# Kernel optimization log

Measured on AMD Instinct MI355X. Metric: run time of the kernel, lower is better.

The kernel has to match this reference:

```python
import jax, jax.numpy as jnp
import numpy as np

B, N, C = 8, 4096, 512
NH, R = 8, 4
EPS = 1e-5

def setup_inputs() -> dict:
    key = jax.random.key(0)
    ks = jax.random.split(key, 6)
    s = lambda k, shape: jax.random.normal(k, shape, jnp.float32) * 0.02
    return {
        'x': jax.random.normal(ks[0], (B, N, C), jnp.float32),
        'Wq': s(ks[1], (C, C)), 'bq': jnp.zeros((C,), jnp.float32),
        'Wkv': s(ks[2], (C, 2 * C)), 'bkv': jnp.zeros((2 * C,), jnp.float32),
        'Wp': s(ks[3], (C, C)), 'bp': jnp.zeros((C,), jnp.float32),
        'Wsr': s(ks[4], (C, C, R, R)), 'bsr': jnp.zeros((C,), jnp.float32),
        'gamma': jnp.ones((C,), jnp.float32), 'beta': jnp.zeros((C,), jnp.float32),
        'H': 64, 'W': 64,
    }

def reference(x, Wq, bq, Wkv, bkv, Wp, bp, Wsr, bsr, gamma, beta, H, W):
    b, n, c = x.shape
    nh = NH
    hd = c // nh
    scale = hd ** -0.5
    # Q projection -> [B, nh, N, hd]
    q = (x @ Wq + bq).reshape(b, n, nh, hd).transpose(0, 2, 1, 3)
    # spatial reduction of KV input: Conv2d(k=stride=R), NCHW
    x_sp = x.transpose(0, 2, 1).reshape(b, c, H, W)
    xr = jax.lax.conv_general_dilated(
        x_sp, Wsr, window_strides=(R, R), padding='VALID',
        dimension_numbers=('NCHW', 'OIHW', 'NCHW')) + bsr[None, :, None, None]
    nr = (H // R) * (W // R)
    xr = xr.reshape(b, c, nr).transpose(0, 2, 1)  # [B, Nr, C]
    # LayerNorm over channels
    mu = xr.mean(-1, keepdims=True)
    var = xr.var(-1, keepdims=True)
    xr = (xr - mu) / jnp.sqrt(var + EPS) * gamma + beta
    # KV projection -> k, v: [B, nh, Nr, hd]
    kv = (xr @ Wkv + bkv).reshape(b, nr, 2, nh, hd)
    k = kv[:, :, 0].transpose(0, 2, 1, 3)
    v = kv[:, :, 1].transpose(0, 2, 1, 3)
    # attention
    attn = jax.nn.softmax(jnp.einsum('bhnd,bhmd->bhnm', q, k) * scale, axis=-1)
    out = jnp.einsum('bhnm,bhmd->bhnd', attn, v).transpose(0, 2, 1, 3).reshape(b, n, c)
    return out @ Wp + bp
```

## Files before the change

kernel.cpp:

```cpp
#include <hip/hip_runtime.h>
#include <stdint.h>

typedef __attribute__((ext_vector_type(8))) short bf16x8;
typedef __attribute__((ext_vector_type(4))) float f32x4;
typedef __attribute__((ext_vector_type(2))) unsigned u32x2;

#define MFMA16(a,b,c) __builtin_amdgcn_mfma_f32_16x16x32_bf16(a,b,c,0,0,0)

typedef const __attribute__((address_space(1))) void GV;
typedef __attribute__((address_space(3))) void LV;

static __device__ __forceinline__ void gload16(const void* g, void* l) {
  __builtin_amdgcn_global_load_lds((GV*)g, (LV*)l, 16, 0, 0);
}

static __device__ __forceinline__ unsigned short f2bf(float f) {
  union { float f; unsigned u; } x; x.f = f;
  unsigned r = x.u + 0x7FFFu + ((x.u >> 16) & 1u);
  return (unsigned short)(r >> 16);
}

static __device__ __forceinline__ float fast_exp2(float x) {
#if __has_builtin(__builtin_amdgcn_exp2f)
  return __builtin_amdgcn_exp2f(x);
#else
  return __expf(x * 0.6931471805599453f);
#endif
}

__global__ __launch_bounds__(256) void pack_x_kernel(
    const float* __restrict__ x, unsigned short* __restrict__ xb) {
  int i = blockIdx.x * 256 + threadIdx.x;
  float4 v = ((const float4*)x)[i];
  unsigned a0 = f2bf(v.x), a1 = f2bf(v.y), a2 = f2bf(v.z), a3 = f2bf(v.w);
  uint2 pk; pk.x = a0 | (a1 << 16); pk.y = a2 | (a3 << 16);
  ((uint2*)xb)[i] = pk;
}

__global__ __launch_bounds__(256) void pack_w_kernel(
    const float* __restrict__ Wq, const float* __restrict__ Wkv,
    const float* __restrict__ Wp, const float* __restrict__ Wsr,
    unsigned short* __restrict__ wqt, unsigned short* __restrict__ wkvt,
    unsigned short* __restrict__ wpt, unsigned short* __restrict__ wsrt) {
  int idx = blockIdx.x * 256 + threadIdx.x;
  if (idx < 262144) {
    int n = idx >> 9, k = idx & 511;
    wqt[idx] = f2bf(Wq[k * 512 + n]);
  } else if (idx < 786432) {
    int j = idx - 262144; int n = j >> 9, k = j & 511;
    wkvt[j] = f2bf(Wkv[k * 1024 + n]);
  } else if (idx < 1048576) {
    int j = idx - 786432; int n = j >> 9, k = j & 511;
    wpt[j] = f2bf(Wp[k * 512 + n]);
  } else {
    int j = idx - 1048576;
    int oc = j >> 13, rem = j & 8191;
    int r12 = rem >> 9, ic = rem & 511;
    wsrt[j] = f2bf(Wsr[oc * 8192 + ic * 16 + r12]);
  }
}

template<int WM, int WN, int MREP, int NREP, int MODE, bool CONV, bool SWZ>
__global__ __launch_bounds__(256) void gemm_bf16(
    const unsigned short* __restrict__ A, const unsigned short* __restrict__ Bt,
    const float* __restrict__ bias, void* __restrict__ outp,
    unsigned short* __restrict__ out_k, unsigned short* __restrict__ out_v,
    int M, int N, int K, int lda, int Ksub) {
  constexpr int BM = WM * MREP * 16;
  constexpr int BN = WN * NREP * 16;
  constexpr int BK = 64;
  constexpr int ABYTES = BM * BK * 2;
  constexpr int BBYTES = BN * BK * 2;
  __shared__ unsigned short lds_a[2 * BM * BK];
  __shared__ unsigned short lds_b[2 * BN * BK];
  const int tid = threadIdx.x;
  const int lane = tid & 63, w = tid >> 6;
  const int wr = w / WN, wc = w % WN;
  const int l15 = lane & 15, lhi = lane >> 4;
  const int xmask = (l15 & 7) << 4;
  const int smask = ((tid >> 3) & 7) << 3;
  int mt, nt_;
  if constexpr (SWZ) {
    int lin = blockIdx.x + blockIdx.y * gridDim.x;
    int nwg = gridDim.x * gridDim.y;
    int cpx = nwg >> 3;
    int s = (lin & 7) * cpx + (lin >> 3);
    int gdy = gridDim.y;
    mt = s / gdy; nt_ = s - mt * gdy;
  } else { mt = blockIdx.x; nt_ = blockIdx.y; }
  const int m0 = mt * BM;
  const int n0 = nt_ * BN;
  const int kbeg = blockIdx.z * Ksub;

  f32x4 acc[MREP][NREP] = {};
  constexpr int AR = ABYTES / 4096;
  constexpr int BR = BBYTES / 4096;
  constexpr int NL = AR + BR;

  auto stage = [&](int buf, int k0) {
    #pragma unroll
    for (int r = 0; r < AR; ++r) {
      int o = r * 4096 + tid * 16;
      int row = o >> 7;
      int kc = (((o & 127) >> 1)) ^ smask;
      const unsigned short* src;
      if constexpr (CONV) {
        int m = m0 + row;
        int bb = m >> 8, pix = m & 255;
        int oh = pix >> 4, ow = pix & 15;
        int r12 = k0 >> 9;
        int icc = (k0 & 511) + kc;
        int r1 = r12 >> 2, r2 = r12 & 3;
        int nn = (oh * 4 + r1) * 64 + ow * 4 + r2;
        src = A + ((size_t)(bb * 4096 + nn)) * 512 + icc;
      } else {
        src = A + (size_t)(m0 + row) * lda + k0 + kc;
      }
      gload16(src, (char*)lds_a + buf * ABYTES + r * 4096 + w * 1024);
    }
    #pragma unroll
    for (int r = 0; r < BR; ++r) {
      int o = r * 4096 + tid * 16;
      int row = o >> 7;
      int kc = (((o & 127) >> 1)) ^ smask;
      const unsigned short* src = Bt + (size_t)(n0 + row) * K + k0 + kc;
      gload16(src, (char*)lds_b + buf * BBYTES + r * 4096 + w * 1024);
    }
  };

  auto waitn = [&]() {
    if constexpr (NL == 4)      asm volatile("s_waitcnt vmcnt(4)" ::: "memory");
    else if constexpr (NL == 6) asm volatile("s_waitcnt vmcnt(6)" ::: "memory");
    else                        asm volatile("s_waitcnt vmcnt(8)" ::: "memory");
  };

  auto compute = [&](int buf) {
    const char* pa = (const char*)lds_a + buf * ABYTES;
    const char* pb = (const char*)lds_b + buf * BBYTES;
    #pragma unroll
    for (int kk = 0; kk < BK; kk += 32) {
      bf16x8 af[MREP], bfr[NREP];
      #pragma unroll
      for (int m = 0; m < MREP; ++m)
        af[m] = *(const bf16x8*)(pa + (wr * MREP * 16 + m * 16 + l15) * (BK * 2)
                                 + (((kk << 1) + (lhi << 4)) ^ xmask));
      #pragma unroll
      for (int n = 0; n < NREP; ++n)
        bfr[n] = *(const bf16x8*)(pb + (wc * NREP * 16 + n * 16 + l15) * (BK * 2)
                                  + (((kk << 1) + (lhi << 4)) ^ xmask));
      __builtin_amdgcn_s_setprio(1);
      #pragma unroll
      for (int m = 0; m < MREP; ++m)
        #pragma unroll
        for (int n = 0; n < NREP; ++n)
          acc[m][n] = MFMA16(af[m], bfr[n], acc[m][n]);
      __builtin_amdgcn_s_setprio(0);
    }
  };

  const int nsteps = Ksub / BK;
  stage(0, kbeg);
  int buf = 0;
  for (int t = 0; t < nsteps; ++t) {
    if (t + 1 < nsteps) {
      stage(buf ^ 1, kbeg + (t + 1) * BK);
      waitn();
    } else {
      asm volatile("s_waitcnt vmcnt(0)" ::: "memory");
    }
    __builtin_amdgcn_s_barrier();
    compute(buf);
    __builtin_amdgcn_s_barrier();
    buf ^= 1;
  }

  #pragma unroll
  for (int m = 0; m < MREP; ++m) {
    #pragma unroll
    for (int n = 0; n < NREP; ++n) {
      #pragma unroll
      for (int r = 0; r < 4; ++r) {
        int gm = m0 + wr * MREP * 16 + m * 16 + lhi * 4 + r;
        int gn = n0 + wc * NREP * 16 + n * 16 + l15;
        if constexpr (MODE == 0) {
          float v = acc[m][n][r] + bias[gn];
          ((float*)outp)[(size_t)gm * N + gn] = v;
        } else if constexpr (MODE == 3) {
          ((float*)outp)[((size_t)blockIdx.z * M + gm) * N + gn] = acc[m][n][r];
        } else if constexpr (MODE == 4) {
          float v = (acc[m][n][r] + bias[gn]) * 0.18033688011112042f;
          int b_ = gm >> 12, n_ = gm & 4095;
          int hh = gn >> 6, d = gn & 63;
          int qt = n_ >> 4, half = d >> 5, dd = d & 31;
          int ln = (n_ & 15) | ((dd >> 3) << 4);
          ((unsigned short*)outp)[(size_t)(b_ * 8 + hh) * 262144 +
              (qt * 2 + half) * 512 + ln * 8 + (d & 7)] = f2bf(v);
        } else {
          float v = acc[m][n][r] + bias[gn];
          unsigned short bv = f2bf(v);
          int bb = gm >> 8, nr = gm & 255;
          if (gn < 512) {
            int hh = gn >> 6, d = gn & 63;
            int t_ = nr >> 4, half = d >> 5, dd = d & 31;
            int ln = (nr & 15) | ((dd >> 3) << 4);
            out_k[(size_t)(bb * 8 + hh) * 16384 +
                  (t_ * 2 + half) * 512 + ln * 8 + (d & 7)] = bv;
          } else {
            int c = gn - 512;
            int hh = c >> 6, d = c & 63;
            int nn = d >> 4, cl = d & 15;
            int ks = nr >> 5, lh = (nr >> 3) & 3;
            out_v[(size_t)(bb * 8 + hh) * 16384 +
                  (nn * 8 + ks) * 512 + (cl | (lh << 4)) * 8 + (nr & 7)] = bv;
          }
        }
      }
    }
  }
}

__global__ __launch_bounds__(64) void ln_kernel(
    const float* __restrict__ part, const float* __restrict__ bsr,
    const float* __restrict__ gamma, const float* __restrict__ beta,
    unsigned short* __restrict__ xln) {
  const int row = blockIdx.x, lane = threadIdx.x;
  float vv[8];
  #pragma unroll
  for (int j = 0; j < 8; ++j) vv[j] = bsr[lane * 8 + j];
  #pragma unroll
  for (int p = 0; p < 4; ++p) {
    const float* pp = part + ((size_t)p * 2048 + row) * 512 + lane * 8;
    float4 a0 = *(const float4*)pp;
    float4 a1 = *(const float4*)(pp + 4);
    vv[0] += a0.x; vv[1] += a0.y; vv[2] += a0.z; vv[3] += a0.w;
    vv[4] += a1.x; vv[5] += a1.y; vv[6] += a1.z; vv[7] += a1.w;
  }
  float s = 0.f, s2 = 0.f;
  #pragma unroll
  for (int j = 0; j < 8; ++j) { s += vv[j]; s2 += vv[j] * vv[j]; }
  #pragma unroll
  for (int m_ = 1; m_ < 64; m_ <<= 1) { s += __shfl_xor(s, m_); s2 += __shfl_xor(s2, m_); }
  float mean = s * (1.f / 512.f);
  float var = s2 * (1.f / 512.f) - mean * mean;
  float inv = rsqrtf(var + 1e-5f);
  #pragma unroll
  for (int j = 0; j < 8; ++j) {
    int c = lane * 8 + j;
    xln[(size_t)row * 512 + c] = f2bf((vv[j] - mean) * inv * gamma[c] + beta[c]);
  }
}

__global__ __launch_bounds__(512, 4) void attn_kernel(
    const unsigned short* __restrict__ qfrag, const unsigned short* __restrict__ kfrag,
    const unsigned short* __restrict__ vfrag, unsigned short* __restrict__ aout) {
  __shared__ unsigned short k_lds[16384];
  __shared__ unsigned short v_lds[16384];
  const int tid = threadIdx.x, lane = tid & 63, w = tid >> 6;
  const int l15 = lane & 15;
  const int b = blockIdx.z, h = blockIdx.y;
  const int bh = b * 8 + h;
  const char* kb_ = (const char*)(kfrag + (size_t)bh * 16384);
  const char* vb_ = (const char*)(vfrag + (size_t)bh * 16384);
  #pragma unroll
  for (int r = 0; r < 4; ++r) {
    gload16(kb_ + r * 8192 + tid * 16, (char*)k_lds + r * 8192 + w * 1024);
    gload16(vb_ + r * 8192 + tid * 16, (char*)v_lds + r * 8192 + w * 1024);
  }
  const int qt = blockIdx.x * 8 + w;
  const unsigned short* qbase = qfrag + (size_t)bh * 262144 + (size_t)qt * 1024;
  bf16x8 qf0 = *(const bf16x8*)(qbase + lane * 8);
  bf16x8 qf1 = *(const bf16x8*)(qbase + 512 + lane * 8);
  __syncthreads();

  f32x4 st[16];
  #pragma unroll
  for (int t = 0; t < 16; ++t) {
    bf16x8 kf0 = *(const bf16x8*)&k_lds[t * 1024 + lane * 8];
    bf16x8 kf1 = *(const bf16x8*)&k_lds[t * 1024 + 512 + lane * 8];
    f32x4 a = {0.f, 0.f, 0.f, 0.f};
    a = MFMA16(kf0, qf0, a);
    a = MFMA16(kf1, qf1, a);
    st[t] = a;
  }

  float sum = 0.f;
  unsigned pk2[16][2];
  #pragma unroll
  for (int t = 0; t < 16; ++t) {
    float p0 = fast_exp2(st[t][0]), p1 = fast_exp2(st[t][1]);
    float p2 = fast_exp2(st[t][2]), p3 = fast_exp2(st[t][3]);
    sum += (p0 + p1) + (p2 + p3);
    unsigned r0, r1;
    asm("v_cvt_pk_bf16_f32 %0, %1, %2" : "=v"(r0) : "v"(p0), "v"(p1));
    asm("v_cvt_pk_bf16_f32 %0, %1, %2" : "=v"(r1) : "v"(p2), "v"(p3));
    pk2[t][0] = r0; pk2[t][1] = r1;
  }
  sum += __shfl_xor(sum, 16);
  sum += __shfl_xor(sum, 32);
  float invs = 1.f / sum;

  const int lhi_ = lane >> 4;
  const int srcA = l15 + (((2 * lhi_) & 3) << 4);
  const int srcB = l15 + (((2 * lhi_ + 1) & 3) << 4);
  const bool hi2 = lhi_ >= 2;
  f32x4 o[4] = {};
  #pragma unroll
  for (int ks = 0; ks < 8; ++ks) {
    union { unsigned u[4]; bf16x8 v; } pu;
    unsigned A0 = __shfl(pk2[2 * ks][0], srcA),     A0b = __shfl(pk2[2 * ks][1], srcA);
    unsigned A1 = __shfl(pk2[2 * ks + 1][0], srcA), A1b = __shfl(pk2[2 * ks + 1][1], srcA);
    unsigned B0 = __shfl(pk2[2 * ks][0], srcB),     B0b = __shfl(pk2[2 * ks][1], srcB);
    unsigned B1 = __shfl(pk2[2 * ks + 1][0], srcB), B1b = __shfl(pk2[2 * ks + 1][1], srcB);
    pu.u[0] = hi2 ? A1 : A0;  pu.u[1] = hi2 ? A1b : A0b;
    pu.u[2] = hi2 ? B1 : B0;  pu.u[3] = hi2 ? B1b : B0b;
    #pragma unroll
    for (int n = 0; n < 4; ++n) {
      bf16x8 vf = *(const bf16x8*)&v_lds[(n * 8 + ks) * 512 + lane * 8];
      o[n] = MFMA16(vf, pu.v, o[n]);
    }
  }

  const int q0 = blockIdx.x * 128;
  const int lhi = lane >> 4;
  #pragma unroll
  for (int n = 0; n < 4; ++n) {
    float a0 = o[n][0] * invs, a1 = o[n][1] * invs;
    float a2 = o[n][2] * invs, a3 = o[n][3] * invs;
    unsigned w0, w1;
    asm("v_cvt_pk_bf16_f32 %0, %1, %2" : "=v"(w0) : "v"(a0), "v"(a1));
    asm("v_cvt_pk_bf16_f32 %0, %1, %2" : "=v"(w1) : "v"(a2), "v"(a3));
    u32x2 pr; pr[0] = w0; pr[1] = w1;
    size_t base = (size_t)(b * 4096 + q0 + w * 16 + l15) * 512 + h * 64 + n * 16 + lhi * 4;
    *(u32x2*)(aout + base) = pr;
  }
}

extern "C" void kernel_launch(void* const* d_in, const int* in_sizes, int n_in,
                              void* d_out, int out_size, void* d_ws, size_t ws_size,
                              hipStream_t stream) {
  const float* x     = (const float*)d_in[0];
  const float* Wq    = (const float*)d_in[1];
  const float* bq    = (const float*)d_in[2];
  const float* Wkv   = (const float*)d_in[3];
  const float* bkv   = (const float*)d_in[4];
  const float* Wp    = (const float*)d_in[5];
  const float* bp    = (const float*)d_in[6];
  const float* Wsr   = (const float*)d_in[7];
  const float* bsr   = (const float*)d_in[8];
  const float* gamma = (const float*)d_in[9];
  const float* beta  = (const float*)d_in[10];

  char* ws = (char*)d_ws;
  unsigned short* xb    = (unsigned short*)(ws + 0);
  float*          part  = (float*)(ws + 33554432);
  unsigned short* qfrag = (unsigned short*)(ws + 33554432);
  unsigned short* wqt   = (unsigned short*)(ws + 67108864);
  unsigned short* wkvt  = (unsigned short*)(ws + 67633152);
  unsigned short* wpt   = (unsigned short*)(ws + 68681728);
  unsigned short* wsrt  = (unsigned short*)(ws + 69206016);
  unsigned short* xln   = (unsigned short*)(ws + 77594624);
  unsigned short* kfrag = (unsigned short*)(ws + 79691776);
  unsigned short* vfrag = (unsigned short*)(ws + 81788928);
  unsigned short* aout  = xb;

  pack_x_kernel<<<16384, 256, 0, stream>>>(x, xb);
  pack_w_kernel<<<20480, 256, 0, stream>>>(Wq, Wkv, Wp, Wsr, wqt, wkvt, wpt, wsrt);
  gemm_bf16<2, 2, 2, 2, 3, true, false><<<dim3(32, 8, 4), 256, 0, stream>>>(
      xb, wsrt, nullptr, part, nullptr, nullptr, 2048, 512, 8192, 512, 2048);
  ln_kernel<<<2048, 64, 0, stream>>>(part, bsr, gamma, beta, xln);
  gemm_bf16<2, 2, 2, 4, 2, false, false><<<dim3(32, 8, 1), 256, 0, stream>>>(
      xln, wkvt, bkv, nullptr, kfrag, vfrag, 2048, 1024, 512, 512, 512);
  gemm_bf16<2, 2, 4, 4, 4, false, true><<<dim3(256, 4, 1), 256, 0, stream>>>(
      xb, wqt, bq, qfrag, nullptr, nullptr, 32768, 512, 512, 512, 512);
  attn_kernel<<<dim3(32, 8, 8), 512, 0, stream>>>(qfrag, kfrag, vfrag, aout);
  gemm_bf16<2, 2, 4, 4, 0, false, true><<<dim3(256, 4, 1), 256, 0, stream>>>(
      aout, wpt, bp, (float*)d_out, nullptr, nullptr, 32768, 512, 512, 512, 512);
}
```

Before: 168.7 us.

## Merge pack kernels, fuse Q and KV projections, retile conv split-K

Combines the x and weight packing into one launch and transposes the weights through LDS tiles so both reads and writes are coalesced. The Q-projection and KV-projection GEMMs now run in one grid with a shared GEMM body. The conv GEMM moves to 128x128 tiles with 8-way split-K and a swizzled block order, so the LayerNorm kernel now sums 8 partials. This cuts launches and strided weight accesses, at the cost of more partial-sum traffic and tighter LDS and register use.

```diff
diff --git a/kernel.cpp b/kernel.cpp
--- a/kernel.cpp
+++ b/kernel.cpp
@@ -28,69 +28,81 @@
 #endif
 }
 
-__global__ __launch_bounds__(256) void pack_x_kernel(
-    const float* __restrict__ x, unsigned short* __restrict__ xb) {
-  int i = blockIdx.x * 256 + threadIdx.x;
-  float4 v = ((const float4*)x)[i];
-  unsigned a0 = f2bf(v.x), a1 = f2bf(v.y), a2 = f2bf(v.z), a3 = f2bf(v.w);
-  uint2 pk; pk.x = a0 | (a1 << 16); pk.y = a2 | (a3 << 16);
-  ((uint2*)xb)[i] = pk;
-}
-
-__global__ __launch_bounds__(256) void pack_w_kernel(
-    const float* __restrict__ Wq, const float* __restrict__ Wkv,
-    const float* __restrict__ Wp, const float* __restrict__ Wsr,
-    unsigned short* __restrict__ wqt, unsigned short* __restrict__ wkvt,
-    unsigned short* __restrict__ wpt, unsigned short* __restrict__ wsrt) {
-  int idx = blockIdx.x * 256 + threadIdx.x;
-  if (idx < 262144) {
-    int n = idx >> 9, k = idx & 511;
-    wqt[idx] = f2bf(Wq[k * 512 + n]);
-  } else if (idx < 786432) {
-    int j = idx - 262144; int n = j >> 9, k = j & 511;
-    wkvt[j] = f2bf(Wkv[k * 1024 + n]);
-  } else if (idx < 1048576) {
-    int j = idx - 786432; int n = j >> 9, k = j & 511;
-    wpt[j] = f2bf(Wp[k * 512 + n]);
-  } else {
-    int j = idx - 1048576;
-    int oc = j >> 13, rem = j & 8191;
-    int r12 = rem >> 9, ic = rem & 511;
-    wsrt[j] = f2bf(Wsr[oc * 8192 + ic * 16 + r12]);
-  }
-}
-
-template<int WM, int WN, int MREP, int NREP, int MODE, bool CONV, bool SWZ>
-__global__ __launch_bounds__(256) void gemm_bf16(
+__global__ __launch_bounds__(256) void pack_all(
+    const float* __restrict__ x, const float* __restrict__ Wq,
+    const float* __restrict__ Wkv, const float* __restrict__ Wp,
+    const float* __restrict__ Wsr,
+    unsigned short* __restrict__ xb, unsigned short* __restrict__ wqt,
+    unsigned short* __restrict__ wkvt, unsigned short* __restrict__ wpt,
+    unsigned short* __restrict__ wsrt) {
+  const int tid = threadIdx.x;
+  int bid = blockIdx.x;
+  if (bid < 16384) {
+    int i = bid * 256 + tid;
+    float4 v = ((const float4*)x)[i];
+    unsigned a0 = f2bf(v.x), a1 = f2bf(v.y), a2 = f2bf(v.z), a3 = f2bf(v.w);
+    uint2 pk; pk.x = a0 | (a1 << 16); pk.y = a2 | (a3 << 16);
+    ((uint2*)xb)[i] = pk;
+    return;
+  }
+  bid -= 16384;
+  __shared__ float lsm[8704];
+
+  auto wtile = [&](const float* __restrict__ W, unsigned short* __restrict__ out,
+                   int ldw, int tr, int tc) {
+    int k0 = tr * 64, n0 = tc * 64;
+    #pragma unroll
+    for (int i = 0; i < 16; ++i) {
+      int idx = i * 256 + tid; int r = idx >> 6, c = idx & 63;
+      lsm[r * 65 + c] = W[(size_t)(k0 + r) * ldw + n0 + c];
+    }
+    __syncthreads();
+    #pragma unroll
+    for (int i = 0; i < 16; ++i) {
+      int idx = i * 256 + tid; int n = idx >> 6, k = idx & 63;
+      out[(size_t)(n0 + n) * 512 + k0 + k] = f2bf(lsm[k * 65 + n]);
+    }
+  };
+
+  if (bid < 64) { wtile(Wq, wqt, 512, bid >> 3, bid & 7); return; }
+  bid -= 64;
+  if (bid < 128) { wtile(Wkv, wkvt, 1024, bid >> 4, bid & 15); return; }
+  bid -= 128;
+  if (bid < 64) { wtile(Wp, wpt, 512, bid >> 3, bid & 7); return; }
+  bid -= 64;
+  int oc = bid;
+  #pragma unroll
+  for (int i = 0; i < 32; ++i) {
+    int idx = i * 256 + tid;
+    lsm[(idx >> 4) * 17 + (idx & 15)] = Wsr[(size_t)oc * 8192 + idx];
+  }
+  __syncthreads();
+  #pragma unroll
+  for (int i = 0; i < 32; ++i) {
+    int idx = i * 256 + tid;
+    int ic = idx & 511, r12 = idx >> 9;
+    wsrt[(size_t)oc * 8192 + idx] = f2bf(lsm[ic * 17 + r12]);
+  }
+}
+
+template<int WM, int WN, int MREP, int NREP, int MODE, bool CONV>
+static __device__ __forceinline__ void gemm_body(
+    unsigned short* lds_a, unsigned short* lds_b,
     const unsigned short* __restrict__ A, const unsigned short* __restrict__ Bt,
     const float* __restrict__ bias, void* __restrict__ outp,
     unsigned short* __restrict__ out_k, unsigned short* __restrict__ out_v,
-    int M, int N, int K, int lda, int Ksub) {
+    int M, int N, int K, int lda, int Ksub, int m0, int n0, int kbeg, int zslice) {
   constexpr int BM = WM * MREP * 16;
   constexpr int BN = WN * NREP * 16;
   constexpr int BK = 64;
   constexpr int ABYTES = BM * BK * 2;
   constexpr int BBYTES = BN * BK * 2;
-  __shared__ unsigned short lds_a[2 * BM * BK];
-  __shared__ unsigned short lds_b[2 * BN * BK];
   const int tid = threadIdx.x;
   const int lane = tid & 63, w = tid >> 6;
   const int wr = w / WN, wc = w % WN;
   const int l15 = lane & 15, lhi = lane >> 4;
   const int xmask = (l15 & 7) << 4;
   const int smask = ((tid >> 3) & 7) << 3;
-  int mt, nt_;
-  if constexpr (SWZ) {
-    int lin = blockIdx.x + blockIdx.y * gridDim.x;
-    int nwg = gridDim.x * gridDim.y;
-    int cpx = nwg >> 3;
-    int s = (lin & 7) * cpx + (lin >> 3);
-    int gdy = gridDim.y;
-    mt = s / gdy; nt_ = s - mt * gdy;
-  } else { mt = blockIdx.x; nt_ = blockIdx.y; }
-  const int m0 = mt * BM;
-  const int n0 = nt_ * BN;
-  const int kbeg = blockIdx.z * Ksub;
 
   f32x4 acc[MREP][NREP] = {};
   constexpr int AR = ABYTES / 4096;
@@ -186,7 +198,7 @@
           float v = acc[m][n][r] + bias[gn];
           ((float*)outp)[(size_t)gm * N + gn] = v;
         } else if constexpr (MODE == 3) {
-          ((float*)outp)[((size_t)blockIdx.z * M + gm) * N + gn] = acc[m][n][r];
+          ((float*)outp)[((size_t)zslice * M + gm) * N + gn] = acc[m][n][r];
         } else if constexpr (MODE == 4) {
           float v = (acc[m][n][r] + bias[gn]) * 0.18033688011112042f;
           int b_ = gm >> 12, n_ = gm & 4095;
@@ -219,6 +231,54 @@
   }
 }
 
+template<int WM, int WN, int MREP, int NREP, int MODE, bool CONV, bool SWZ>
+__global__ __launch_bounds__(256) void gemm_bf16(
+    const unsigned short* __restrict__ A, const unsigned short* __restrict__ Bt,
+    const float* __restrict__ bias, void* __restrict__ outp,
+    unsigned short* __restrict__ out_k, unsigned short* __restrict__ out_v,
+    int M, int N, int K, int lda, int Ksub) {
+  constexpr int BM = WM * MREP * 16;
+  constexpr int BN = WN * NREP * 16;
+  __shared__ unsigned short lds_a[2 * BM * 64];
+  __shared__ unsigned short lds_b[2 * BN * 64];
+  int mt, nt_;
+  if constexpr (SWZ) {
+    int lin = blockIdx.x + blockIdx.y * gridDim.x;
+    int nwg = gridDim.x * gridDim.y;
+    int cpx = nwg >> 3;
+    int s = (lin & 7) * cpx + (lin >> 3);
+    int gdy = gridDim.y;
+    mt = s / gdy; nt_ = s - mt * gdy;
+  } else { mt = blockIdx.x; nt_ = blockIdx.y; }
+  gemm_body<WM, WN, MREP, NREP, MODE, CONV>(
+      lds_a, lds_b, A, Bt, bias, outp, out_k, out_v,
+      M, N, K, lda, Ksub, mt * BM, nt_ * BN, blockIdx.z * Ksub, blockIdx.z);
+}
+
+__global__ __launch_bounds__(256) void proj_fused(
+    const unsigned short* __restrict__ xb, const unsigned short* __restrict__ wqt,
+    const float* __restrict__ bq, unsigned short* __restrict__ qfrag,
+    const unsigned short* __restrict__ xln, const unsigned short* __restrict__ wkvt,
+    const float* __restrict__ bkv, unsigned short* __restrict__ kfrag,
+    unsigned short* __restrict__ vfrag) {
+  __shared__ unsigned short lds_a[2 * 128 * 64];
+  __shared__ unsigned short lds_b[2 * 128 * 64];
+  int bx = blockIdx.x;
+  if (bx < 1024) {
+    int s = (bx & 7) * 128 + (bx >> 3);
+    int mt = s >> 2, nt_ = s & 3;
+    gemm_body<2, 2, 4, 4, 4, false>(
+        lds_a, lds_b, xb, wqt, bq, qfrag, nullptr, nullptr,
+        32768, 512, 512, 512, 512, mt * 128, nt_ * 128, 0, 0);
+  } else {
+    int b2 = bx - 1024;
+    int mt = b2 >> 3, nt_ = b2 & 7;
+    gemm_body<2, 2, 4, 4, 2, false>(
+        lds_a, lds_b, xln, wkvt, bkv, nullptr, kfrag, vfrag,
+        2048, 1024, 512, 512, 512, mt * 128, nt_ * 128, 0, 0);
+  }
+}
+
 __global__ __launch_bounds__(64) void ln_kernel(
     const float* __restrict__ part, const float* __restrict__ bsr,
     const float* __restrict__ gamma, const float* __restrict__ beta,
@@ -228,7 +288,7 @@
   #pragma unroll
   for (int j = 0; j < 8; ++j) vv[j] = bsr[lane * 8 + j];
   #pragma unroll
-  for (int p = 0; p < 4; ++p) {
+  for (int p = 0; p < 8; ++p) {
     const float* pp = part + ((size_t)p * 2048 + row) * 512 + lane * 8;
     float4 a0 = *(const float4*)pp;
     float4 a1 = *(const float4*)(pp + 4);
@@ -363,15 +423,11 @@
   unsigned short* vfrag = (unsigned short*)(ws + 81788928);
   unsigned short* aout  = xb;
 
-  pack_x_kernel<<<16384, 256, 0, stream>>>(x, xb);
-  pack_w_kernel<<<20480, 256, 0, stream>>>(Wq, Wkv, Wp, Wsr, wqt, wkvt, wpt, wsrt);
-  gemm_bf16<2, 2, 2, 2, 3, true, false><<<dim3(32, 8, 4), 256, 0, stream>>>(
-      xb, wsrt, nullptr, part, nullptr, nullptr, 2048, 512, 8192, 512, 2048);
+  pack_all<<<17152, 256, 0, stream>>>(x, Wq, Wkv, Wp, Wsr, xb, wqt, wkvt, wpt, wsrt);
+  gemm_bf16<2, 2, 4, 4, 3, true, true><<<dim3(16, 4, 8), 256, 0, stream>>>(
+      xb, wsrt, nullptr, part, nullptr, nullptr, 2048, 512, 8192, 512, 1024);
   ln_kernel<<<2048, 64, 0, stream>>>(part, bsr, gamma, beta, xln);
-  gemm_bf16<2, 2, 2, 4, 2, false, false><<<dim3(32, 8, 1), 256, 0, stream>>>(
-      xln, wkvt, bkv, nullptr, kfrag, vfrag, 2048, 1024, 512, 512, 512);
-  gemm_bf16<2, 2, 4, 4, 4, false, true><<<dim3(256, 4, 1), 256, 0, stream>>>(
-      xb, wqt, bq, qfrag, nullptr, nullptr, 32768, 512, 512, 512, 512);
+  proj_fused<<<1152, 256, 0, stream>>>(xb, wqt, bq, qfrag, xln, wkvt, bkv, kfrag, vfrag);
   attn_kernel<<<dim3(32, 8, 8), 512, 0, stream>>>(qfrag, kfrag, vfrag, aout);
   gemm_bf16<2, 2, 4, 4, 0, false, true><<<dim3(256, 4, 1), 256, 0, stream>>>(
       aout, wpt, bp, (float*)d_out, nullptr, nullptr, 32768, 512, 512, 512, 512);
```

Result: faster. 154.3 us (-8.6%).
